# Optimization experiments

Hardware: AMD Instinct MI355X
Metric: run time of the kernel (lower is better)

The kernel has to match this reference:

```python
import jax, jax.numpy as jnp
import numpy as np

S = 30.0  # scale
M = 0.4   # margin
IN_FEATURES = 512
OUT_FEATURES = 100000
BATCH = 1024
EPS = 1e-12


def setup_inputs() -> dict:
    key = jax.random.key(0)
    kx, kw, kl = jax.random.split(key, 3)
    x = jax.random.normal(kx, (BATCH, IN_FEATURES), dtype=jnp.float32)
    labels = jax.random.randint(kl, (BATCH,), 0, OUT_FEATURES, dtype=jnp.int64)
    # nn.Linear(in, out, bias=False).weight has shape [out, in]
    W = jax.random.normal(kw, (OUT_FEATURES, IN_FEATURES), dtype=jnp.float32) * (1.0 / np.sqrt(IN_FEATURES))
    return {"x": x, "labels": labels, "W": W}


def reference(x, labels, W):
    # Faithful to the torch module (training path, 1D labels):
    # the `for W in parameters(): W = F.normalize(W)` loop is a no-op in torch
    # (rebinds a local name), so W is used UNNORMALIZED; only x is normalized.
    x_n = x / jnp.maximum(jnp.linalg.norm(x, axis=1, keepdims=True), EPS)
    wf = jnp.einsum('bd,cd->bc', x_n, W)  # [B, C] logits
    target_logit = jnp.take_along_axis(wf, labels[:, None], axis=1)[:, 0]  # wf[i, labels[i]]
    numerator = S * (target_logit - M)
    # excl = row of wf with the target column removed -> masked exp-sum
    one_hot = labels[:, None] == jnp.arange(wf.shape[1])[None, :]
    excl_sum = jnp.sum(jnp.where(one_hot, 0.0, jnp.exp(S * wf)), axis=1)
    denominator = jnp.exp(numerator) + excl_sum
    L = numerator - jnp.log(denominator)
    return -jnp.mean(L)
```

## Files before the change

kernel.cpp:

```cpp
#include <hip/hip_runtime.h>
#include <hip/hip_bf16.h>

#define BATCH 1024
#define DIM 512
#define NCLS 100000
#define SCALE 30.0f
#define MARGIN 0.4f
#define BM 128
#define BN 64
#define BK 64
#define NT ((NCLS + BN - 1) / BN)

typedef __bf16 bf16x8 __attribute__((ext_vector_type(8)));
typedef __bf16 bf16x4 __attribute__((ext_vector_type(4)));
typedef float f32x4 __attribute__((ext_vector_type(4)));

__global__ __launch_bounds__(256) void k_norm(const float* __restrict__ x,
                                              __bf16* __restrict__ xb) {
    int row  = blockIdx.x * 4 + (threadIdx.x >> 6);
    int lane = threadIdx.x & 63;
    const float* xr = x + (size_t)row * DIM;
    float4 v0 = *reinterpret_cast<const float4*>(xr + lane * 4);
    float4 v1 = *reinterpret_cast<const float4*>(xr + 256 + lane * 4);
    float ss = v0.x*v0.x + v0.y*v0.y + v0.z*v0.z + v0.w*v0.w
             + v1.x*v1.x + v1.y*v1.y + v1.z*v1.z + v1.w*v1.w;
#pragma unroll
    for (int m = 1; m < 64; m <<= 1) ss += __shfl_xor(ss, m);
    float inv = 1.0f / fmaxf(sqrtf(ss), 1e-12f);
    bf16x4 o0 = { (__bf16)(v0.x*inv), (__bf16)(v0.y*inv), (__bf16)(v0.z*inv), (__bf16)(v0.w*inv) };
    bf16x4 o1 = { (__bf16)(v1.x*inv), (__bf16)(v1.y*inv), (__bf16)(v1.z*inv), (__bf16)(v1.w*inv) };
    *reinterpret_cast<bf16x4*>(xb + (size_t)row * DIM + lane * 4)       = o0;
    *reinterpret_cast<bf16x4*>(xb + (size_t)row * DIM + 256 + lane * 4) = o1;
}

__global__ __launch_bounds__(256) void k_main(const __bf16* __restrict__ xb,
                                              const float* __restrict__ W,
                                              const int* __restrict__ lab32,
                                              float* __restrict__ part,
                                              float* __restrict__ tgt) {
    int bid = blockIdx.x;
    int ct  = bid >> 3;
    int rt  = bid & 7;
    int tid = threadIdx.x;
    int wid = tid >> 6;
    int lane = tid & 63;
    int rowBase = rt * BM;
    int colBase = ct * BN;

    __shared__ __bf16 Asm[BM * BK];
    __shared__ __bf16 Bsm[BN * BK];
    __shared__ int    slab[BM];
    __shared__ int    sflag;

    if (tid < 64) {
        int o = 0;
        for (int i = lane; i < 512; i += 64) o |= lab32[2 * i + 1];
#pragma unroll
        for (int m = 1; m < 64; m <<= 1) o |= __shfl_xor(o, m);
        if (lane == 0) sflag = o;
    }
    __syncthreads();
    bool is64 = (sflag == 0);
    if (tid < BM) slab[tid] = is64 ? lab32[2 * (rowBase + tid)] : lab32[rowBase + tid];

    f32x4 acc[2][4];
#pragma unroll
    for (int m = 0; m < 2; m++)
#pragma unroll
        for (int n = 0; n < 4; n++) acc[m][n] = (f32x4){0.f, 0.f, 0.f, 0.f};

    for (int k0 = 0; k0 < DIM; k0 += BK) {
        __syncthreads();
#pragma unroll
        for (int i = 0; i < 4; i++) {
            int idx = i * 2048 + tid * 8;
            int r = idx >> 6, k = idx & 63;
            bf16x8 v = *reinterpret_cast<const bf16x8*>(xb + (size_t)(rowBase + r) * DIM + k0 + k);
            int byte = (r * 128 + k * 2) ^ ((r & 7) << 4);
            *reinterpret_cast<bf16x8*>(reinterpret_cast<char*>(Asm) + byte) = v;
        }
#pragma unroll
        for (int i = 0; i < 4; i++) {
            int idx = i * 1024 + tid * 4;
            int r = idx >> 6, k = idx & 63;
            int c = colBase + r;
            float4 v = (c < NCLS) ? *reinterpret_cast<const float4*>(W + (size_t)c * DIM + k0 + k)
                                  : make_float4(0.f, 0.f, 0.f, 0.f);
            bf16x4 h = { (__bf16)v.x, (__bf16)v.y, (__bf16)v.z, (__bf16)v.w };
            int byte = (r * 128 + k * 2) ^ ((r & 7) << 4);
            *reinterpret_cast<bf16x4*>(reinterpret_cast<char*>(Bsm) + byte) = h;
        }
        __syncthreads();
#pragma unroll
        for (int ks = 0; ks < 2; ks++) {
            bf16x8 a[2], b[4];
            int kk = (ks * 32 + (lane >> 4) * 8) * 2;
#pragma unroll
            for (int m = 0; m < 2; m++) {
                int r = wid * 32 + m * 16 + (lane & 15);
                int byte = (r * 128 + kk) ^ ((r & 7) << 4);
                a[m] = *reinterpret_cast<const bf16x8*>(reinterpret_cast<const char*>(Asm) + byte);
            }
#pragma unroll
            for (int n = 0; n < 4; n++) {
                int r = n * 16 + (lane & 15);
                int byte = (r * 128 + kk) ^ ((r & 7) << 4);
                b[n] = *reinterpret_cast<const bf16x8*>(reinterpret_cast<const char*>(Bsm) + byte);
            }
#pragma unroll
            for (int m = 0; m < 2; m++)
#pragma unroll
                for (int n = 0; n < 4; n++)
                    acc[m][n] = __builtin_amdgcn_mfma_f32_16x16x32_bf16(a[m], b[n], acc[m][n], 0, 0, 0);
        }
    }

#pragma unroll
    for (int m = 0; m < 2; m++) {
#pragma unroll
        for (int r = 0; r < 4; r++) {
            int trow = wid * 32 + m * 16 + (lane >> 4) * 4 + r;
            int grow = rowBase + trow;
            int lb = slab[trow];
            float s = 0.f;
#pragma unroll
            for (int n = 0; n < 4; n++) {
                int gcol = colBase + n * 16 + (lane & 15);
                float v = acc[m][n][r];
                if (gcol == lb) tgt[grow] = v;
                if (gcol < NCLS && gcol != lb) s += __expf(SCALE * v);
            }
#pragma unroll
            for (int mm = 1; mm < 16; mm <<= 1) s += __shfl_xor(s, mm);
            if ((lane & 15) == 0) part[(size_t)grow * NT + ct] = s;
        }
    }
}

__global__ __launch_bounds__(256) void k_row(const float* __restrict__ part,
                                             const float* __restrict__ tgt,
                                             float* __restrict__ Lrow) {
    int row = blockIdx.x;
    int tid = threadIdx.x;
    float s = 0.f;
    for (int t = tid; t < NT; t += 256) s += part[(size_t)row * NT + t];
#pragma unroll
    for (int m = 1; m < 64; m <<= 1) s += __shfl_xor(s, m);
    __shared__ float red[4];
    if ((tid & 63) == 0) red[tid >> 6] = s;
    __syncthreads();
    if (tid == 0) {
        float excl = red[0] + red[1] + red[2] + red[3];
        float num = SCALE * (tgt[row] - MARGIN);
        float den = __expf(num) + excl;
        Lrow[row] = num - logf(den);
    }
}

__global__ __launch_bounds__(1024) void k_final(const float* __restrict__ Lrow,
                                                float* __restrict__ out) {
    int tid = threadIdx.x;
    float v = Lrow[tid];
#pragma unroll
    for (int m = 1; m < 64; m <<= 1) v += __shfl_xor(v, m);
    __shared__ float red[16];
    if ((tid & 63) == 0) red[tid >> 6] = v;
    __syncthreads();
    if (tid == 0) {
        float s = 0.f;
#pragma unroll
        for (int i = 0; i < 16; i++) s += red[i];
        out[0] = -s / (float)BATCH;
    }
}

extern "C" void kernel_launch(void* const* d_in, const int* in_sizes, int n_in,
                              void* d_out, int out_size, void* d_ws, size_t ws_size,
                              hipStream_t stream) {
    const float* x   = (const float*)d_in[0];
    const int*   lab = (const int*)d_in[1];
    const float* W   = (const float*)d_in[2];
    float* out = (float*)d_out;

    char* ws = (char*)d_ws;
    __bf16* xb  = (__bf16*)ws;
    float*  part = (float*)(ws + (1 << 20));
    float*  tgt  = (float*)(ws + (1 << 20) + (size_t)BATCH * NT * 4);
    float*  Lrow = tgt + BATCH;

    k_norm <<<BATCH / 4, 256, 0, stream>>>(x, xb);
    k_main <<<NT * 8,    256, 0, stream>>>(xb, W, lab, part, tgt);
    k_row  <<<BATCH,     256, 0, stream>>>(part, tgt, Lrow);
    k_final<<<1,        1024, 0, stream>>>(Lrow, out);
}
```

Baseline: 586.9 us.

## Process full batch per block, stream A from global, double-buffer W tiles

Each block now covers all 1024 rows for a 64-column slice, with 8 waves each owning 128 rows. A fragments are loaded straight from global/L2 into registers, and W is staged through a double-buffered shared-memory tile with a single barrier per K step. This means each W element is read from HBM and converted to bf16 once instead of eight times. The trade-off is a much larger accumulator set per thread (32 f32x4), which lowers occupancy, plus repeated L2 reads of xb by every block.

```diff
diff --git a/kernel.cpp b/kernel.cpp
--- a/kernel.cpp
+++ b/kernel.cpp
@@ -6,9 +6,10 @@
 #define NCLS 100000
 #define SCALE 30.0f
 #define MARGIN 0.4f
-#define BM 128
+#define BM 1024
 #define BN 64
-#define BK 64
+#define BK 32
+#define KSTEPS (DIM / BK)
 #define NT ((NCLS + BN - 1) / BN)
 
 typedef __bf16 bf16x8 __attribute__((ext_vector_type(8)));
@@ -33,24 +34,21 @@
     *reinterpret_cast<bf16x4*>(xb + (size_t)row * DIM + 256 + lane * 4) = o1;
 }
 
-__global__ __launch_bounds__(256) void k_main(const __bf16* __restrict__ xb,
+__global__ __launch_bounds__(512) void k_main(const __bf16* __restrict__ xb,
                                               const float* __restrict__ W,
                                               const int* __restrict__ lab32,
                                               float* __restrict__ part,
                                               float* __restrict__ tgt) {
-    int bid = blockIdx.x;
-    int ct  = bid >> 3;
-    int rt  = bid & 7;
-    int tid = threadIdx.x;
-    int wid = tid >> 6;
-    int lane = tid & 63;
-    int rowBase = rt * BM;
-    int colBase = ct * BN;
-
-    __shared__ __bf16 Asm[BM * BK];
-    __shared__ __bf16 Bsm[BN * BK];
-    __shared__ int    slab[BM];
-    __shared__ int    sflag;
+    const int ct      = blockIdx.x;
+    const int colBase = ct * BN;
+    const int tid     = threadIdx.x;
+    const int wid     = tid >> 6;
+    const int lane    = tid & 63;
+    const int wrow    = wid * 128;
+
+    __shared__ __align__(16) __bf16 Bs[2][4][BN][8];
+    __shared__ int slab[BATCH];
+    __shared__ int sflag;
 
     if (tid < 64) {
         int o = 0;
@@ -60,79 +58,103 @@
         if (lane == 0) sflag = o;
     }
     __syncthreads();
-    bool is64 = (sflag == 0);
-    if (tid < BM) slab[tid] = is64 ? lab32[2 * (rowBase + tid)] : lab32[rowBase + tid];
-
-    f32x4 acc[2][4];
-#pragma unroll
-    for (int m = 0; m < 2; m++)
+    const bool is64 = (sflag == 0);
+    for (int i = tid; i < BATCH; i += 512) slab[i] = is64 ? lab32[2 * i] : lab32[i];
+
+    f32x4 acc[8][4];
+#pragma unroll
+    for (int m = 0; m < 8; m++)
 #pragma unroll
         for (int n = 0; n < 4; n++) acc[m][n] = (f32x4){0.f, 0.f, 0.f, 0.f};
 
-    for (int k0 = 0; k0 < DIM; k0 += BK) {
+    const char* aBase = (const char*)xb
+                      + (size_t)(wrow + (lane & 15)) * (DIM * 2)
+                      + (lane >> 4) * 16;
+
+    auto loadA = [&](int t, bf16x8* a) {
+        const char* p = aBase + t * (BK * 2);
+#pragma unroll
+        for (int m = 0; m < 8; m++)
+            a[m] = *reinterpret_cast<const bf16x8*>(p + m * 16 * (DIM * 2));
+    };
+
+    const int skg = tid >> 6;
+    const int sc  = tid & 63;
+    const int sgc = colBase + sc;
+    const bool sact = (tid < 256) && (sgc < NCLS);
+    const float* wBase = W + (size_t)sgc * DIM + skg * 8;
+
+    auto stageLoad = [&](int t, float4& f0, float4& f1) {
+        if (sact) {
+            const float* p = wBase + t * BK;
+            f0 = *reinterpret_cast<const float4*>(p);
+            f1 = *reinterpret_cast<const float4*>(p + 4);
+        } else {
+            f0 = make_float4(0.f, 0.f, 0.f, 0.f);
+            f1 = f0;
+        }
+    };
+    auto stageWrite = [&](int buf, const float4& f0, const float4& f1) {
+        if (tid < 256) {
+            bf16x8 h = { (__bf16)f0.x, (__bf16)f0.y, (__bf16)f0.z, (__bf16)f0.w,
+                         (__bf16)f1.x, (__bf16)f1.y, (__bf16)f1.z, (__bf16)f1.w };
+            *reinterpret_cast<bf16x8*>(&Bs[buf][skg][sc][0]) = h;
+        }
+    };
+
+    bf16x8 aA[8], aB[8];
+
+    loadA(0, aA);
+    {
+        float4 f0, f1;
+        stageLoad(0, f0, f1);
+        stageWrite(0, f0, f1);
+    }
+    __syncthreads();
+
+    auto iter = [&](int t, bf16x8* aC, bf16x8* aN) {
+        const int cur = t & 1;
+        float4 f0, f1;
+        if (t + 1 < KSTEPS) {
+            stageLoad(t + 1, f0, f1);
+            loadA(t + 1, aN);
+        }
+        bf16x8 b[4];
+#pragma unroll
+        for (int n = 0; n < 4; n++)
+            b[n] = *reinterpret_cast<const bf16x8*>(&Bs[cur][lane >> 4][n * 16 + (lane & 15)][0]);
+#pragma unroll
+        for (int m = 0; m < 8; m++)
+#pragma unroll
+            for (int n = 0; n < 4; n++)
+                acc[m][n] = __builtin_amdgcn_mfma_f32_16x16x32_bf16(aC[m], b[n], acc[m][n], 0, 0, 0);
+        if (t + 1 < KSTEPS) stageWrite(cur ^ 1, f0, f1);
         __syncthreads();
-#pragma unroll
-        for (int i = 0; i < 4; i++) {
-            int idx = i * 2048 + tid * 8;
-            int r = idx >> 6, k = idx & 63;
-            bf16x8 v = *reinterpret_cast<const bf16x8*>(xb + (size_t)(rowBase + r) * DIM + k0 + k);
-            int byte = (r * 128 + k * 2) ^ ((r & 7) << 4);
-            *reinterpret_cast<bf16x8*>(reinterpret_cast<char*>(Asm) + byte) = v;
-        }
-#pragma unroll
-        for (int i = 0; i < 4; i++) {
-            int idx = i * 1024 + tid * 4;
-            int r = idx >> 6, k = idx & 63;
-            int c = colBase + r;
-            float4 v = (c < NCLS) ? *reinterpret_cast<const float4*>(W + (size_t)c * DIM + k0 + k)
-                                  : make_float4(0.f, 0.f, 0.f, 0.f);
-            bf16x4 h = { (__bf16)v.x, (__bf16)v.y, (__bf16)v.z, (__bf16)v.w };
-            int byte = (r * 128 + k * 2) ^ ((r & 7) << 4);
-            *reinterpret_cast<bf16x4*>(reinterpret_cast<char*>(Bsm) + byte) = h;
-        }
-        __syncthreads();
-#pragma unroll
-        for (int ks = 0; ks < 2; ks++) {
-            bf16x8 a[2], b[4];
-            int kk = (ks * 32 + (lane >> 4) * 8) * 2;
-#pragma unroll
-            for (int m = 0; m < 2; m++) {
-                int r = wid * 32 + m * 16 + (lane & 15);
-                int byte = (r * 128 + kk) ^ ((r & 7) << 4);
-                a[m] = *reinterpret_cast<const bf16x8*>(reinterpret_cast<const char*>(Asm) + byte);
-            }
-#pragma unroll
-            for (int n = 0; n < 4; n++) {
-                int r = n * 16 + (lane & 15);
-                int byte = (r * 128 + kk) ^ ((r & 7) << 4);
-                b[n] = *reinterpret_cast<const bf16x8*>(reinterpret_cast<const char*>(Bsm) + byte);
-            }
-#pragma unroll
-            for (int m = 0; m < 2; m++)
-#pragma unroll
-                for (int n = 0; n < 4; n++)
-                    acc[m][n] = __builtin_amdgcn_mfma_f32_16x16x32_bf16(a[m], b[n], acc[m][n], 0, 0, 0);
-        }
-    }
-
-#pragma unroll
-    for (int m = 0; m < 2; m++) {
+    };
+
+#pragma unroll
+    for (int th = 0; th < KSTEPS / 2; th++) {
+        iter(2 * th,     aA, aB);
+        iter(2 * th + 1, aB, aA);
+    }
+
+#pragma unroll
+    for (int m = 0; m < 8; m++) {
 #pragma unroll
         for (int r = 0; r < 4; r++) {
-            int trow = wid * 32 + m * 16 + (lane >> 4) * 4 + r;
-            int grow = rowBase + trow;
+            int trow = wrow + m * 16 + (lane >> 4) * 4 + r;
             int lb = slab[trow];
             float s = 0.f;
 #pragma unroll
             for (int n = 0; n < 4; n++) {
                 int gcol = colBase + n * 16 + (lane & 15);
                 float v = acc[m][n][r];
-                if (gcol == lb) tgt[grow] = v;
+                if (gcol == lb) tgt[trow] = v;
                 if (gcol < NCLS && gcol != lb) s += __expf(SCALE * v);
             }
 #pragma unroll
             for (int mm = 1; mm < 16; mm <<= 1) s += __shfl_xor(s, mm);
-            if ((lane & 15) == 0) part[(size_t)grow * NT + ct] = s;
+            if ((lane & 15) == 0) part[(size_t)trow * NT + ct] = s;
         }
     }
 }
@@ -189,7 +211,7 @@
     float*  Lrow = tgt + BATCH;
 
     k_norm <<<BATCH / 4, 256, 0, stream>>>(x, xb);
-    k_main <<<NT * 8,    256, 0, stream>>>(xb, W, lab, part, tgt);
+    k_main <<<NT,        512, 0, stream>>>(xb, W, lab, part, tgt);
     k_row  <<<BATCH,     256, 0, stream>>>(part, tgt, Lrow);
     k_final<<<1,        1024, 0, stream>>>(Lrow, out);
 }
```

New measurement: 623.0 us. 6.1% more time.

## Double-buffer W tiles, load A fragments directly, and swizzle block order

Applied to the files above, without the earlier changes.

The main GEMM kernel now prefetches the next K-step of W into registers while the MFMAs run on the current one, and stores it into a double-buffered LDS layout. That layout is [k-group][col][8], so B fragments are read without an XOR swizzle. The normalized x fragments are loaded straight from global memory into registers instead of being staged through LDS, which removes the A shared-memory traffic. The block index is remapped so groups of 8 column tiles are spread across the 8 row tiles, which should improve L2 reuse of W. In exchange the kernel uses more registers, issues redundant global loads of x across waves, and launches some padding blocks that exit early.

```diff
diff --git a/kernel.cpp b/kernel.cpp
--- a/kernel.cpp
+++ b/kernel.cpp
@@ -9,7 +9,9 @@
 #define BM 128
 #define BN 64
 #define BK 64
+#define KSTEPS (DIM / BK)
 #define NT ((NCLS + BN - 1) / BN)
+#define GRID_MAIN (8 * 8 * 196)
 
 typedef __bf16 bf16x8 __attribute__((ext_vector_type(8)));
 typedef __bf16 bf16x4 __attribute__((ext_vector_type(4)));
@@ -38,19 +40,19 @@
                                               const int* __restrict__ lab32,
                                               float* __restrict__ part,
                                               float* __restrict__ tgt) {
-    int bid = blockIdx.x;
-    int ct  = bid >> 3;
-    int rt  = bid & 7;
-    int tid = threadIdx.x;
-    int wid = tid >> 6;
-    int lane = tid & 63;
-    int rowBase = rt * BM;
-    int colBase = ct * BN;
-
-    __shared__ __bf16 Asm[BM * BK];
-    __shared__ __bf16 Bsm[BN * BK];
-    __shared__ int    slab[BM];
-    __shared__ int    sflag;
+    const int idx = blockIdx.x;
+    const int ct  = (idx & 7) + ((idx >> 6) << 3);
+    if (ct >= NT) return;
+    const int rt  = (idx >> 3) & 7;
+    const int colBase = ct * BN;
+    const int rowBase = rt * BM;
+    const int tid  = threadIdx.x;
+    const int wid  = tid >> 6;
+    const int lane = tid & 63;
+
+    __shared__ __align__(16) __bf16 Bs[2][8][BN][8];
+    __shared__ int slab[BM];
+    __shared__ int sflag;
 
     if (tid < 64) {
         int o = 0;
@@ -60,7 +62,7 @@
         if (lane == 0) sflag = o;
     }
     __syncthreads();
-    bool is64 = (sflag == 0);
+    const bool is64 = (sflag == 0);
     if (tid < BM) slab[tid] = is64 ? lab32[2 * (rowBase + tid)] : lab32[rowBase + tid];
 
     f32x4 acc[2][4];
@@ -69,50 +71,67 @@
 #pragma unroll
         for (int n = 0; n < 4; n++) acc[m][n] = (f32x4){0.f, 0.f, 0.f, 0.f};
 
-    for (int k0 = 0; k0 < DIM; k0 += BK) {
+    const char* aB = (const char*)xb
+                   + (size_t)(rowBase + wid * 32 + (lane & 15)) * (DIM * 2)
+                   + (lane >> 4) * 16;
+
+    const int scol = tid & 63;
+    const int skq  = tid >> 6;
+    const int sgc  = colBase + scol;
+    const bool sok = (sgc < NCLS);
+    const float* wB = W + (size_t)(sok ? sgc : 0) * DIM + skq * 16;
+
+    auto LDA = [&](int t, bf16x8* a) {
+#pragma unroll
+        for (int ks = 0; ks < 2; ks++)
+#pragma unroll
+            for (int m = 0; m < 2; m++)
+                a[ks * 2 + m] = *reinterpret_cast<const bf16x8*>(
+                    aB + (size_t)m * 16 * (DIM * 2) + ks * 64 + t * (BK * 2));
+    };
+    auto LDB = [&](int t, float4* f) {
+#pragma unroll
+        for (int i = 0; i < 4; i++)
+            f[i] = sok ? *reinterpret_cast<const float4*>(wB + t * BK + i * 4)
+                       : make_float4(0.f, 0.f, 0.f, 0.f);
+    };
+    auto STB = [&](int buf, const float4* f) {
+        bf16x8 h0 = { (__bf16)f[0].x, (__bf16)f[0].y, (__bf16)f[0].z, (__bf16)f[0].w,
+                      (__bf16)f[1].x, (__bf16)f[1].y, (__bf16)f[1].z, (__bf16)f[1].w };
+        bf16x8 h1 = { (__bf16)f[2].x, (__bf16)f[2].y, (__bf16)f[2].z, (__bf16)f[2].w,
+                      (__bf16)f[3].x, (__bf16)f[3].y, (__bf16)f[3].z, (__bf16)f[3].w };
+        *reinterpret_cast<bf16x8*>(&Bs[buf][skq * 2][scol][0])     = h0;
+        *reinterpret_cast<bf16x8*>(&Bs[buf][skq * 2 + 1][scol][0]) = h1;
+    };
+    auto CMP = [&](int buf, const bf16x8* a) {
+#pragma unroll
+        for (int ks = 0; ks < 2; ks++)
+#pragma unroll
+            for (int n = 0; n < 4; n++) {
+                bf16x8 b = *reinterpret_cast<const bf16x8*>(
+                    &Bs[buf][ks * 4 + (lane >> 4)][n * 16 + (lane & 15)][0]);
+                acc[0][n] = __builtin_amdgcn_mfma_f32_16x16x32_bf16(a[ks * 2 + 0], b, acc[0][n], 0, 0, 0);
+                acc[1][n] = __builtin_amdgcn_mfma_f32_16x16x32_bf16(a[ks * 2 + 1], b, acc[1][n], 0, 0, 0);
+            }
+    };
+
+    bf16x8 a0[4], a1[4];
+    float4 f0[4], f1[4];
+
+    LDA(0, a0); LDB(0, f0); STB(0, f0);
+    __syncthreads();
+#pragma unroll
+    for (int th = 0; th < KSTEPS / 2; th++) {
+        const int t = 2 * th;
+        LDB(t + 1, f1);
+        LDA(t + 1, a1);
+        CMP(0, a0);
+        STB(1, f1);
         __syncthreads();
-#pragma unroll
-        for (int i = 0; i < 4; i++) {
-            int idx = i * 2048 + tid * 8;
-            int r = idx >> 6, k = idx & 63;
-            bf16x8 v = *reinterpret_cast<const bf16x8*>(xb + (size_t)(rowBase + r) * DIM + k0 + k);
-            int byte = (r * 128 + k * 2) ^ ((r & 7) << 4);
-            *reinterpret_cast<bf16x8*>(reinterpret_cast<char*>(Asm) + byte) = v;
-        }
-#pragma unroll
-        for (int i = 0; i < 4; i++) {
-            int idx = i * 1024 + tid * 4;
-            int r = idx >> 6, k = idx & 63;
-            int c = colBase + r;
-            float4 v = (c < NCLS) ? *reinterpret_cast<const float4*>(W + (size_t)c * DIM + k0 + k)
-                                  : make_float4(0.f, 0.f, 0.f, 0.f);
-            bf16x4 h = { (__bf16)v.x, (__bf16)v.y, (__bf16)v.z, (__bf16)v.w };
-            int byte = (r * 128 + k * 2) ^ ((r & 7) << 4);
-            *reinterpret_cast<bf16x4*>(reinterpret_cast<char*>(Bsm) + byte) = h;
-        }
+        if (th < KSTEPS / 2 - 1) { LDB(t + 2, f0); LDA(t + 2, a0); }
+        CMP(1, a1);
+        if (th < KSTEPS / 2 - 1) STB(0, f0);
         __syncthreads();
-#pragma unroll
-        for (int ks = 0; ks < 2; ks++) {
-            bf16x8 a[2], b[4];
-            int kk = (ks * 32 + (lane >> 4) * 8) * 2;
-#pragma unroll
-            for (int m = 0; m < 2; m++) {
-                int r = wid * 32 + m * 16 + (lane & 15);
-                int byte = (r * 128 + kk) ^ ((r & 7) << 4);
-                a[m] = *reinterpret_cast<const bf16x8*>(reinterpret_cast<const char*>(Asm) + byte);
-            }
-#pragma unroll
-            for (int n = 0; n < 4; n++) {
-                int r = n * 16 + (lane & 15);
-                int byte = (r * 128 + kk) ^ ((r & 7) << 4);
-                b[n] = *reinterpret_cast<const bf16x8*>(reinterpret_cast<const char*>(Bsm) + byte);
-            }
-#pragma unroll
-            for (int m = 0; m < 2; m++)
-#pragma unroll
-                for (int n = 0; n < 4; n++)
-                    acc[m][n] = __builtin_amdgcn_mfma_f32_16x16x32_bf16(a[m], b[n], acc[m][n], 0, 0, 0);
-        }
     }
 
 #pragma unroll
@@ -189,7 +208,7 @@
     float*  Lrow = tgt + BATCH;
 
     k_norm <<<BATCH / 4, 256, 0, stream>>>(x, xb);
-    k_main <<<NT * 8,    256, 0, stream>>>(xb, W, lab, part, tgt);
+    k_main <<<GRID_MAIN, 256, 0, stream>>>(xb, W, lab, part, tgt);
     k_row  <<<BATCH,     256, 0, stream>>>(part, tgt, Lrow);
     k_final<<<1,        1024, 0, stream>>>(Lrow, out);
 }
```

Result: slower. 613.3 us (+4.5%).
